# Optimization experiments

Measured on AMD Instinct MI355X. Metric: run time of the kernel, lower is better.

The kernel has to match this reference:

```python
import jax, jax.numpy as jnp
import numpy as np


def setup_inputs() -> dict:
    key = jax.random.key(0)
    k1, k2, k3 = jax.random.split(key, 3)
    B, L, D = 8, 4096, 320
    CB_DIM, N_BOOKS = 16, 8192
    input_values = jax.random.normal(k1, (B, L, D), dtype=jnp.float32)
    # mask all ones -> static masked-select shape N = B*L
    mask_time_indices = jnp.ones((B, L), dtype=jnp.int32)
    # xavier_uniform for Linear(D -> CB_DIM, bias=False): limit = sqrt(6/(fan_in+fan_out))
    limit = float(np.sqrt(6.0 / (D + CB_DIM)))
    proj_weight = jax.random.uniform(k2, (CB_DIM, D), dtype=jnp.float32, minval=-limit, maxval=limit)
    code_book = jax.random.normal(k3, (N_BOOKS, CB_DIM), dtype=jnp.float32)
    return {"input_values": input_values, "mask_time_indices": mask_time_indices,
            "proj_weight": proj_weight, "code_book": code_book}


def reference(input_values, mask_time_indices, proj_weight, code_book):
    # input_values: [B, L, D]; mask is all-ones so masked select == flatten (static shape N=B*L)
    B, L, D = input_values.shape
    flat = input_values.reshape(B * L, D)  # [N, D]
    targets = flat @ proj_weight.T  # [N, cb_dim]  (random projection, no bias)
    # argmin over Euclidean norm == argmin over squared distance (monotone),
    # expanded form avoids the [N, n_books, cb_dim] broadcast intermediate.
    t2 = jnp.sum(targets * targets, axis=-1, keepdims=True)        # [N, 1]
    c2 = jnp.sum(code_book * code_book, axis=-1)                   # [n_books]
    d2 = t2 - 2.0 * (targets @ code_book.T) + c2                   # [N, n_books]
    labels = jnp.argmin(d2, axis=-1)                               # [N]
    return labels
```

## Files before the change

### kernel.cpp

```cpp
#include <hip/hip_runtime.h>

#define N_ROWS 32768
#define D_IN 320
#define CB 16
#define N_BOOKS 8192

typedef __attribute__((ext_vector_type(8))) short bf16x8;
typedef __attribute__((ext_vector_type(4))) float f32x4;
#define MFMA __builtin_amdgcn_mfma_f32_16x16x32_bf16
#define AS1 __attribute__((address_space(1)))
#define AS3 __attribute__((address_space(3)))

__device__ __forceinline__ unsigned short bf16rn(float f) {
  unsigned u = __float_as_uint(f);
  u += 0x7fffu + ((u >> 16) & 1u);
  return (unsigned short)(u >> 16);
}
__device__ __forceinline__ float bf16tof(unsigned short h) {
  return __uint_as_float(((unsigned)h) << 16);
}
__device__ __forceinline__ void gload_lds16(const short* g, short* l) {
  __builtin_amdgcn_global_load_lds((const AS1 unsigned int*)g, (AS3 unsigned int*)l, 16, 0, 0);
}

__global__ __launch_bounds__(256, 2) void proj_prep_kernel(
    const float* __restrict__ x, const float* __restrict__ w, short* __restrict__ tsplit,
    const float* __restrict__ cbk, short* __restrict__ bfrag, float* __restrict__ nh_g,
    int* __restrict__ ctr) {
  __shared__ __align__(16) short wfrag[3][10][64][8];
  __shared__ __align__(16) float xs[2][64 * 36];
  const int tid = threadIdx.x;

  if (blockIdx.x >= 512) {
    const int bid = blockIdx.x - 512;
    if (bid == 0 && tid == 0) *ctr = 0;
    const int j = bid * 256 + tid;
    const float4* src = (const float4*)(cbk + (size_t)j * CB);
    float4 a = src[0], b = src[1], c = src[2], d = src[3];
    float ce[16] = {a.x, a.y, a.z, a.w, b.x, b.y, b.z, b.w,
                    c.x, c.y, c.z, c.w, d.x, d.y, d.z, d.w};
    short c1[16], c2[16];
    double s = 0.0;
#pragma unroll
    for (int i = 0; i < 16; i++) {
      s += (double)ce[i] * (double)ce[i];
      unsigned short x1 = bf16rn(ce[i]);
      float r1 = ce[i] - bf16tof(x1);
      unsigned short x2 = bf16rn(r1);
      c1[i] = (short)x1; c2[i] = (short)x2;
    }
    nh_g[j] = (float)(-0.5 * s);
    bf16x8 lo1, hi1, lo2, hi2;
#pragma unroll
    for (int i = 0; i < 8; i++) {
      lo1[i] = c1[i]; hi1[i] = c1[i + 8];
      lo2[i] = c2[i]; hi2[i] = c2[i + 8];
    }
    const int bt = j >> 4, n = j & 15;
    short* base = bfrag + (size_t)bt * 1024;
    *(bf16x8*)(base + (0 * 16 + n) * 8) = lo1;
    *(bf16x8*)(base + (1 * 16 + n) * 8) = hi1;
    *(bf16x8*)(base + (2 * 16 + n) * 8) = lo1;
    *(bf16x8*)(base + (3 * 16 + n) * 8) = hi1;
    *(bf16x8*)(base + 512 + (0 * 16 + n) * 8) = lo2;
    *(bf16x8*)(base + 512 + (1 * 16 + n) * 8) = hi2;
    *(bf16x8*)(base + 512 + (2 * 16 + n) * 8) = lo2;
    *(bf16x8*)(base + 512 + (3 * 16 + n) * 8) = hi2;
    return;
  }

  const int lane = tid & 63;
  const int wv = tid >> 6;

  for (int i = tid; i < D_IN * CB; i += 256) {
    int d = i >> 4, o = i & 15;
    float f = w[o * D_IN + d];
    unsigned short h1 = bf16rn(f);
    float r1 = f - bf16tof(h1);
    unsigned short h2 = bf16rn(r1);
    float r2 = r1 - bf16tof(h2);
    unsigned short h3 = bf16rn(r2);
    int c = d >> 5, qq = (d >> 3) & 3, pos = d & 7;
    int ln = qq * 16 + o;
    wfrag[0][c][ln][pos] = (short)h1;
    wfrag[1][c][ln][pos] = (short)h2;
    wfrag[2][c][ln][pos] = (short)h3;
  }

  const float* xblk = x + (size_t)blockIdx.x * 64 * D_IN;
  {
    int row = tid >> 2, k0 = (tid & 3) * 8;
    float4 v0 = *(const float4*)(xblk + row * D_IN + k0);
    float4 v1 = *(const float4*)(xblk + row * D_IN + k0 + 4);
    *(float4*)&xs[0][row * 36 + k0] = v0;
    *(float4*)&xs[0][row * 36 + k0 + 4] = v1;
  }
  __syncthreads();

  const int m = lane & 15, q = lane >> 4;
  f32x4 g1 = {0.f, 0.f, 0.f, 0.f}, g2 = {0.f, 0.f, 0.f, 0.f}, g3 = {0.f, 0.f, 0.f, 0.f};
  for (int c = 0; c < 10; c++) {
    const int buf = c & 1;
    if (c < 9) {
      int row = tid >> 2, k0 = (tid & 3) * 8;
      float4 v0 = *(const float4*)(xblk + row * D_IN + (c + 1) * 32 + k0);
      float4 v1 = *(const float4*)(xblk + row * D_IN + (c + 1) * 32 + k0 + 4);
      *(float4*)&xs[buf ^ 1][row * 36 + k0] = v0;
      *(float4*)&xs[buf ^ 1][row * 36 + k0 + 4] = v1;
    }
    const float* xp = &xs[buf][(wv * 16 + m) * 36 + q * 8];
    float4 xa = *(const float4*)xp;
    float4 xb = *(const float4*)(xp + 4);
    float xe[8] = {xa.x, xa.y, xa.z, xa.w, xb.x, xb.y, xb.z, xb.w};
    bf16x8 a1, a2, a3;
#pragma unroll
    for (int j = 0; j < 8; j++) {
      unsigned short h1 = bf16rn(xe[j]);
      float r1 = xe[j] - bf16tof(h1);
      unsigned short h2 = bf16rn(r1);
      float r2 = r1 - bf16tof(h2);
      unsigned short h3 = bf16rn(r2);
      a1[j] = (short)h1; a2[j] = (short)h2; a3[j] = (short)h3;
    }
    bf16x8 b1 = *(const bf16x8*)wfrag[0][c][lane];
    bf16x8 b2 = *(const bf16x8*)wfrag[1][c][lane];
    bf16x8 b3 = *(const bf16x8*)wfrag[2][c][lane];
    g1 = MFMA(a1, b1, g1, 0, 0, 0);
    g2 = MFMA(a2, b1, g2, 0, 0, 0);
    g2 = MFMA(a1, b2, g2, 0, 0, 0);
    g3 = MFMA(a3, b1, g3, 0, 0, 0);
    g3 = MFMA(a1, b3, g3, 0, 0, 0);
    g3 = MFMA(a2, b2, g3, 0, 0, 0);
    __syncthreads();
  }

  float* tl = (float*)xs;
#pragma unroll
  for (int r = 0; r < 4; r++) {
    double t = (double)g1[r] + ((double)g2[r] + (double)g3[r]);
    tl[(wv * 16 + q * 4 + r) * 17 + m] = (float)t;
  }
  __syncthreads();
  {
    int row_l = tid >> 2, p = tid & 3;
    short h1[4], h2[4], h3[4];
#pragma unroll
    for (int i = 0; i < 4; i++) {
      float f = tl[row_l * 17 + p * 4 + i];
      unsigned short a = bf16rn(f);
      float r1 = f - bf16tof(a);
      unsigned short b = bf16rn(r1);
      float r2 = r1 - bf16tof(b);
      unsigned short cc = bf16rn(r2);
      h1[i] = (short)a; h2[i] = (short)b; h3[i] = (short)cc;
    }
    size_t base = (size_t)(blockIdx.x * 64 + row_l) * 48;
    *(short4*)(tsplit + base + p * 4) = make_short4(h1[0], h1[1], h1[2], h1[3]);
    *(short4*)(tsplit + base + 16 + p * 4) = make_short4(h2[0], h2[1], h2[2], h2[3]);
    *(short4*)(tsplit + base + 32 + p * 4) = make_short4(h3[0], h3[1], h3[2], h3[3]);
  }
}

#define SC_H 8

__global__ __launch_bounds__(512, 2) void score_kernel(const short* __restrict__ tsplit,
                                                       const short* __restrict__ bfrag,
                                                       const float* __restrict__ nh_g,
                                                       float4* __restrict__ cand) {
  __shared__ __align__(16) short ldsb[3][8192];
  __shared__ float ldsnh[1024];
  const int tid = threadIdx.x;
  const int lane = tid & 63;
  const int wv = tid >> 6;
  const int m = lane & 15, q = lane >> 4;
  const int rb = blockIdx.x & 127;
  const int h = blockIdx.x >> 7;
  const int rowbase = rb * 256;

  bf16x8 A12[2];
#pragma unroll
  for (int rt = 0; rt < 2; rt++) {
    int row = rowbase + wv * 32 + rt * 16 + m;
    A12[rt] = *(const bf16x8*)(tsplit + (size_t)row * 48 + q * 8);
  }
  for (int i = tid; i < 1024; i += 512) ldsnh[i] = nh_g[h * 1024 + i];

  const short* gw = bfrag + (size_t)h * 65536 + wv * 1024 + lane * 8;
  gload_lds16(gw, &ldsb[0][wv * 1024]);
  gload_lds16(gw + 512, &ldsb[0][wv * 1024 + 512]);

  const unsigned qmask = 0xFFFFFFC0u;
  float s1[2][4], s2[2][4];
#pragma unroll
  for (int rt = 0; rt < 2; rt++)
#pragma unroll
    for (int r = 0; r < 4; r++) { s1[rt][r] = -3.4e38f; s2[rt][r] = -3.4e38f; }

  __syncthreads();

  for (int sc = 0; sc < 8; sc++) {
    if (sc < 7) {
      const short* gs = gw + (sc + 1) * 8192;
      short* ld = &ldsb[(sc + 1) % 3][wv * 1024];
      gload_lds16(gs, ld);
      gload_lds16(gs + 512, ld + 512);
      asm volatile("s_waitcnt vmcnt(2)" ::: "memory");
    } else {
      asm volatile("s_waitcnt vmcnt(0)" ::: "memory");
    }
    __builtin_amdgcn_s_barrier();
    asm volatile("" ::: "memory");
    const short* bufp = &ldsb[sc % 3][0];
#pragma unroll
    for (int bt = 0; bt < 8; bt++) {
      const short* bp = bufp + bt * 1024;
      bf16x8 b1 = *(const bf16x8*)(bp + lane * 8);
      bf16x8 b2 = *(const bf16x8*)(bp + 512 + lane * 8);
      const int btg = sc * 8 + bt;
      float nh0 = ldsnh[btg * 16 + m];
      f32x4 ci = {nh0, nh0, nh0, nh0};
      const unsigned tagv = (unsigned)(63 - btg);
#pragma unroll
      for (int rt = 0; rt < 2; rt++) {
        f32x4 acc = MFMA(A12[rt], b1, ci, 0, 0, 0);
        acc = MFMA(A12[rt], b2, acc, 0, 0, 0);
#pragma unroll
        for (int r = 0; r < 4; r++) {
          float vq = __uint_as_float((__float_as_uint(acc[r]) & qmask) | tagv);
          s2[rt][r] = __builtin_amdgcn_fmed3f(vq, s1[rt][r], s2[rt][r]);
          s1[rt][r] = fmaxf(s1[rt][r], vq);
        }
      }
    }
  }

#pragma unroll
  for (int rt = 0; rt < 2; rt++)
#pragma unroll
    for (int r = 0; r < 4; r++) {
      float s1v = s1[rt][r], s2v = s2[rt][r];
      const float ps1 = s1v;
#pragma unroll
      for (int msk = 1; msk <= 8; msk <<= 1) {
        float o1 = __shfl_xor(s1v, msk);
        float o2 = __shfl_xor(s2v, msk);
        s2v = __builtin_amdgcn_fmed3f(s1v, o1, fmaxf(s2v, o2));
        s1v = fmaxf(s1v, o1);
      }
      unsigned long long bal = __ballot(ps1 == s1v);
      unsigned grp = (unsigned)((bal >> (q * 16)) & 0xFFFFull);
      int mwin = __builtin_ctz(grp | 0x10000u);
      int btwin = 63 - (int)(__float_as_uint(s1v) & 63u);
      int col = h * 1024 + btwin * 16 + mwin;
      if (m == 0) {
        int row = rowbase + wv * 32 + rt * 16 + q * 4 + r;
        cand[(size_t)h * N_ROWS + row] = make_float4(s1v, s2v, __int_as_float(col), 0.f);
      }
    }
}

#define MARGIN_EPS 1.0e-3f

__global__ __launch_bounds__(256) void merge_flag_kernel(const float4* __restrict__ cand,
                                                         int* __restrict__ out,
                                                         int* __restrict__ list,
                                                         int* __restrict__ ctr) {
  const int r = blockIdx.x * 256 + threadIdx.x;
  float S1 = -3.4e38f, S2 = -3.4e38f;
  int I = 0;
#pragma unroll
  for (int h = 0; h < SC_H; h++) {
    float4 v = cand[(size_t)h * N_ROWS + r];
    if (v.x > S1) {
      S2 = fmaxf(S1, v.y); S1 = v.x; I = __float_as_int(v.z);
    } else {
      S2 = fmaxf(S2, v.x);
    }
  }
  out[r] = I;
  if (S1 - S2 < MARGIN_EPS) {
    int slot = atomicAdd(ctr, 1);
    list[slot] = r;
  }
}

__global__ __launch_bounds__(256) void rescore_kernel(const int* __restrict__ list,
                                                      const int* __restrict__ ctr,
                                                      const float* __restrict__ x,
                                                      const float* __restrict__ w,
                                                      const float* __restrict__ codebook,
                                                      int* __restrict__ out) {
  __shared__ double ps[16][17];
  __shared__ double tsh[16];
  __shared__ double rs[256];
  __shared__ int ri[256];
  const int tid = threadIdx.x;
  const int total = ctr[0];

  for (int it = blockIdx.x; it < total; it += gridDim.x) {
    const int row = list[it];
    {
      int o = tid & 15, c = tid >> 4;
      double p = 0.0;
      for (int k = 0; k < 20; k++) {
        int d = c * 20 + k;
        p = fma((double)x[(size_t)row * D_IN + d], (double)w[o * D_IN + d], p);
      }
      ps[c][o] = p;
    }
    __syncthreads();
    if (tid < 16) {
      double t = 0.0;
      for (int c = 0; c < 16; c++) t += ps[c][tid];
      tsh[tid] = t;
    }
    __syncthreads();
    double t[16];
#pragma unroll
    for (int i = 0; i < 16; i++) t[i] = tsh[i];
    double bs = -1.0e300;
    int bi = 0;
    for (int j = tid; j < N_BOOKS; j += 256) {
      const float* cp = codebook + (size_t)j * CB;
      double dot = 0.0, cc = 0.0;
#pragma unroll
      for (int i = 0; i < 16; i++) {
        double cv = (double)cp[i];
        dot = fma(t[i], cv, dot);
        cc = fma(cv, cv, cc);
      }
      double mv = dot - 0.5 * cc;
      if (mv > bs) { bs = mv; bi = j; }
    }
    rs[tid] = bs; ri[tid] = bi;
    __syncthreads();
    for (int s = 128; s > 0; s >>= 1) {
      if (tid < s) {
        double os = rs[tid + s]; int oi = ri[tid + s];
        if (os > rs[tid] || (os == rs[tid] && oi < ri[tid])) { rs[tid] = os; ri[tid] = oi; }
      }
      __syncthreads();
    }
    if (tid == 0) out[row] = ri[0];
    __syncthreads();
  }
}

extern "C" void kernel_launch(void* const* d_in, const int* in_sizes, int n_in,
                              void* d_out, int out_size, void* d_ws, size_t ws_size,
                              hipStream_t stream) {
  (void)in_sizes; (void)n_in; (void)out_size; (void)ws_size;
  const float* x = (const float*)d_in[0];
  const float* w = (const float*)d_in[2];
  const float* codebook = (const float*)d_in[3];

  char* ws = (char*)d_ws;
  short* tsplit = (short*)(ws);
  short* bfrag = (short*)(ws + (3 << 20));
  float* nh_g = (float*)(ws + (4 << 20));
  int* list = (int*)(ws + 4231168);
  int* ctr = (int*)(ws + 4362240);
  float4* cand = (float4*)(ws + (5 << 20));
  int* out = (int*)d_out;

  proj_prep_kernel<<<512 + N_BOOKS / 256, 256, 0, stream>>>(x, w, tsplit, codebook, bfrag,
                                                            nh_g, ctr);
  score_kernel<<<128 * SC_H, 512, 0, stream>>>(tsplit, bfrag, nh_g, cand);
  merge_flag_kernel<<<N_ROWS / 256, 256, 0, stream>>>(cand, out, list, ctr);
  rescore_kernel<<<512, 256, 0, stream>>>(list, ctr, x, w, codebook, out);
}
```

Before: 175.7 us.

## Switch score kernel to 32x32x16 MFMA with compact codebook fragment layout

Replaces the 16x16x32 MFMA score loop, which used K-padded duplicated codebook fragments, with 32x32x16 bf16 MFMAs over 32 rows by 32 codes per wave. The codebook fragment buffer halves because the duplicated copies are dropped, and the tag field in the packed argmax key shrinks from 6 to 5 bits. The aim is to remove the wasted duplicate K work and halve the codebook traffic into LDS. In exchange there are 16 accumulators per lane, a wider shuffle reduction, and one less bit of score precision in the packed key.

```diff
diff --git a/kernel.cpp b/kernel.cpp
--- a/kernel.cpp
+++ b/kernel.cpp
@@ -7,7 +7,9 @@
 
 typedef __attribute__((ext_vector_type(8))) short bf16x8;
 typedef __attribute__((ext_vector_type(4))) float f32x4;
+typedef __attribute__((ext_vector_type(16))) float f32x16;
 #define MFMA __builtin_amdgcn_mfma_f32_16x16x32_bf16
+#define MFMA32 __builtin_amdgcn_mfma_f32_32x32x16_bf16
 #define AS1 __attribute__((address_space(1)))
 #define AS3 __attribute__((address_space(3)))
 
@@ -56,16 +58,12 @@
       lo1[i] = c1[i]; hi1[i] = c1[i + 8];
       lo2[i] = c2[i]; hi2[i] = c2[i + 8];
     }
-    const int bt = j >> 4, n = j & 15;
+    const int bt = j >> 5, n = j & 31;
     short* base = bfrag + (size_t)bt * 1024;
-    *(bf16x8*)(base + (0 * 16 + n) * 8) = lo1;
-    *(bf16x8*)(base + (1 * 16 + n) * 8) = hi1;
-    *(bf16x8*)(base + (2 * 16 + n) * 8) = lo1;
-    *(bf16x8*)(base + (3 * 16 + n) * 8) = hi1;
-    *(bf16x8*)(base + 512 + (0 * 16 + n) * 8) = lo2;
-    *(bf16x8*)(base + 512 + (1 * 16 + n) * 8) = hi2;
-    *(bf16x8*)(base + 512 + (2 * 16 + n) * 8) = lo2;
-    *(bf16x8*)(base + 512 + (3 * 16 + n) * 8) = hi2;
+    *(bf16x8*)(base + n * 8) = lo1;
+    *(bf16x8*)(base + n * 8 + 256) = hi1;
+    *(bf16x8*)(base + 512 + n * 8) = lo2;
+    *(bf16x8*)(base + 512 + n * 8 + 256) = hi2;
     return;
   }
 
@@ -172,34 +170,33 @@
   const int tid = threadIdx.x;
   const int lane = tid & 63;
   const int wv = tid >> 6;
-  const int m = lane & 15, q = lane >> 4;
+  const int half = lane >> 5;
   const int rb = blockIdx.x & 127;
   const int h = blockIdx.x >> 7;
   const int rowbase = rb * 256;
 
-  bf16x8 A12[2];
-#pragma unroll
-  for (int rt = 0; rt < 2; rt++) {
-    int row = rowbase + wv * 32 + rt * 16 + m;
-    A12[rt] = *(const bf16x8*)(tsplit + (size_t)row * 48 + q * 8);
+  bf16x8 A1, A2;
+  {
+    const int row = rowbase + wv * 32 + (lane & 31);
+    const short* tp = tsplit + (size_t)row * 48;
+    A1 = *(const bf16x8*)(tp + half * 8);
+    A2 = *(const bf16x8*)(tp + 16 + half * 8);
   }
   for (int i = tid; i < 1024; i += 512) ldsnh[i] = nh_g[h * 1024 + i];
 
-  const short* gw = bfrag + (size_t)h * 65536 + wv * 1024 + lane * 8;
+  const short* gw = bfrag + (size_t)h * 32768 + wv * 1024 + lane * 8;
   gload_lds16(gw, &ldsb[0][wv * 1024]);
   gload_lds16(gw + 512, &ldsb[0][wv * 1024 + 512]);
 
-  const unsigned qmask = 0xFFFFFFC0u;
-  float s1[2][4], s2[2][4];
-#pragma unroll
-  for (int rt = 0; rt < 2; rt++)
-#pragma unroll
-    for (int r = 0; r < 4; r++) { s1[rt][r] = -3.4e38f; s2[rt][r] = -3.4e38f; }
+  const unsigned qmask = 0xFFFFFFE0u;
+  float s1[16], s2[16];
+#pragma unroll
+  for (int r = 0; r < 16; r++) { s1[r] = -3.4e38f; s2[r] = -3.4e38f; }
 
   __syncthreads();
 
-  for (int sc = 0; sc < 8; sc++) {
-    if (sc < 7) {
+  for (int sc = 0; sc < 4; sc++) {
+    if (sc < 3) {
       const short* gs = gw + (sc + 1) * 8192;
       short* ld = &ldsb[(sc + 1) % 3][wv * 1024];
       gload_lds16(gs, ld);
@@ -212,51 +209,50 @@
     asm volatile("" ::: "memory");
     const short* bufp = &ldsb[sc % 3][0];
 #pragma unroll
-    for (int bt = 0; bt < 8; bt++) {
-      const short* bp = bufp + bt * 1024;
-      bf16x8 b1 = *(const bf16x8*)(bp + lane * 8);
-      bf16x8 b2 = *(const bf16x8*)(bp + 512 + lane * 8);
-      const int btg = sc * 8 + bt;
-      float nh0 = ldsnh[btg * 16 + m];
-      f32x4 ci = {nh0, nh0, nh0, nh0};
-      const unsigned tagv = (unsigned)(63 - btg);
-#pragma unroll
-      for (int rt = 0; rt < 2; rt++) {
-        f32x4 acc = MFMA(A12[rt], b1, ci, 0, 0, 0);
-        acc = MFMA(A12[rt], b2, acc, 0, 0, 0);
-#pragma unroll
-        for (int r = 0; r < 4; r++) {
-          float vq = __uint_as_float((__float_as_uint(acc[r]) & qmask) | tagv);
-          s2[rt][r] = __builtin_amdgcn_fmed3f(vq, s1[rt][r], s2[rt][r]);
-          s1[rt][r] = fmaxf(s1[rt][r], vq);
-        }
+    for (int t = 0; t < 8; t++) {
+      const short* bp = bufp + t * 1024;
+      bf16x8 B1 = *(const bf16x8*)(bp + lane * 8);
+      bf16x8 B2 = *(const bf16x8*)(bp + 512 + lane * 8);
+      const int btg = sc * 8 + t;
+      float nh0 = ldsnh[btg * 32 + (lane & 31)];
+      f32x16 acc;
+#pragma unroll
+      for (int r = 0; r < 16; r++) acc[r] = nh0;
+      acc = MFMA32(A2, B2, acc, 0, 0, 0);
+      acc = MFMA32(A2, B1, acc, 0, 0, 0);
+      acc = MFMA32(A1, B2, acc, 0, 0, 0);
+      acc = MFMA32(A1, B1, acc, 0, 0, 0);
+      const unsigned tagv = (unsigned)(31 - btg);
+#pragma unroll
+      for (int r = 0; r < 16; r++) {
+        float vq = __uint_as_float((__float_as_uint(acc[r]) & qmask) | tagv);
+        s2[r] = __builtin_amdgcn_fmed3f(vq, s1[r], s2[r]);
+        s1[r] = fmaxf(s1[r], vq);
       }
     }
   }
 
 #pragma unroll
-  for (int rt = 0; rt < 2; rt++)
-#pragma unroll
-    for (int r = 0; r < 4; r++) {
-      float s1v = s1[rt][r], s2v = s2[rt][r];
-      const float ps1 = s1v;
-#pragma unroll
-      for (int msk = 1; msk <= 8; msk <<= 1) {
-        float o1 = __shfl_xor(s1v, msk);
-        float o2 = __shfl_xor(s2v, msk);
-        s2v = __builtin_amdgcn_fmed3f(s1v, o1, fmaxf(s2v, o2));
-        s1v = fmaxf(s1v, o1);
-      }
-      unsigned long long bal = __ballot(ps1 == s1v);
-      unsigned grp = (unsigned)((bal >> (q * 16)) & 0xFFFFull);
-      int mwin = __builtin_ctz(grp | 0x10000u);
-      int btwin = 63 - (int)(__float_as_uint(s1v) & 63u);
-      int col = h * 1024 + btwin * 16 + mwin;
-      if (m == 0) {
-        int row = rowbase + wv * 32 + rt * 16 + q * 4 + r;
-        cand[(size_t)h * N_ROWS + row] = make_float4(s1v, s2v, __int_as_float(col), 0.f);
-      }
-    }
+  for (int r = 0; r < 16; r++) {
+    float s1v = s1[r], s2v = s2[r];
+    const float ps1 = s1v;
+#pragma unroll
+    for (int msk = 1; msk <= 16; msk <<= 1) {
+      float o1 = __shfl_xor(s1v, msk);
+      float o2 = __shfl_xor(s2v, msk);
+      s2v = __builtin_amdgcn_fmed3f(s1v, o1, fmaxf(s2v, o2));
+      s1v = fmaxf(s1v, o1);
+    }
+    unsigned long long bal = __ballot(ps1 == s1v);
+    unsigned long long grp = (bal >> (half * 32)) & 0xFFFFFFFFull;
+    int nwin = (int)__builtin_ctzll(grp | 0x100000000ull);
+    int btwin = 31 - (int)(__float_as_uint(s1v) & 31u);
+    int col = h * 1024 + btwin * 32 + nwin;
+    if ((lane & 31) == 0) {
+      int row = rowbase + wv * 32 + (r & 3) + 8 * (r >> 2) + 4 * half;
+      cand[(size_t)h * N_ROWS + row] = make_float4(s1v, s2v, __int_as_float(col), 0.f);
+    }
+  }
 }
 
 #define MARGIN_EPS 1.0e-3f
```

New measurement: 182.7 us. 3.9% more time.
